# Kernel tuning notes

Measured on AMD Instinct MI355X. Metric: run time of the kernel, lower is better.

## Reference

```python
import jax, jax.numpy as jnp
import numpy as np

B, S, H, W, C = 1, 14, 56, 56, 192
WS = 7            # cubic window
SH = 3            # shift
HEADS = 6
HD = C // HEADS
N = WS ** 3       # 343 tokens per window
NW = (S // WS) * (H // WS) * (W // WS)  # 128 windows
SCALE = HD ** -0.5
HID = 4 * C
TBL = (2 * WS - 1) ** 3  # 2197


def _rel_index():
    # faithful to torch: meshgrid with indexing='xy' and the (3*ws-1)/(2*ws-1) strides
    c = np.stack(np.meshgrid(np.arange(WS), np.arange(WS), np.arange(WS), indexing='xy'))
    f = c.reshape(3, -1)                      # (3, N)
    r = (f[:, :, None] - f[:, None, :]).transpose(1, 2, 0)  # (N, N, 3)
    r = r + (WS - 1)
    r[..., 0] *= 3 * WS - 1
    r[..., 1] *= 2 * WS - 1
    return jnp.asarray(r.sum(-1), dtype=jnp.int32)  # (N, N)

REL_IDX = _rel_index()


def _ln(x, g, b):
    m = x.mean(-1, keepdims=True)
    v = ((x - m) ** 2).mean(-1, keepdims=True)
    return (x - m) * jax.lax.rsqrt(v + 1e-5) * g + b


def _partition(x):  # (B,S,H,W,C) -> (B*nW, N, C)
    x = x.reshape(B, S // WS, WS, H // WS, WS, W // WS, WS, C)
    x = x.transpose(0, 1, 3, 5, 2, 4, 6, 7)
    return x.reshape(-1, N, C)


def _reverse(w):  # (B*nW, N, C) -> (B,S,H,W,C)
    x = w.reshape(B, S // WS, H // WS, W // WS, WS, WS, WS, C)
    x = x.transpose(0, 1, 4, 2, 5, 3, 6, 7)
    return x.reshape(B, S, H, W, C)


def setup_inputs() -> dict:
    key = jax.random.key(0)
    ks = jax.random.split(key, 16)
    L = S * H * W
    p = lambda k, shp, s=0.02: (jax.random.normal(k, shp, dtype=jnp.float32) * s)
    return {
        'x': jax.random.normal(ks[0], (B, L, C), dtype=jnp.float32),
        'mask_matrix': jax.random.normal(ks[1], (NW, N, N), dtype=jnp.float32),
        'skip': jax.random.normal(ks[2], (B, L, C), dtype=jnp.float32),
        'x_up': jax.random.normal(ks[3], (B, L, C), dtype=jnp.float32),
        'norm1_g': jnp.ones((C,), jnp.float32),
        'norm1_b': jnp.zeros((C,), jnp.float32),
        'kv_w': p(ks[4], (C, 2 * C)),
        'kv_b': jnp.zeros((2 * C,), jnp.float32),
        'rel_bias_table': p(ks[5], (TBL, HEADS)),
        'proj_w': p(ks[6], (C, C)),
        'proj_b': jnp.zeros((C,), jnp.float32),
        'norm2_g': jnp.ones((C,), jnp.float32),
        'norm2_b': jnp.zeros((C,), jnp.float32),
        'fc1_w': p(ks[7], (C, HID)),
        'fc1_b': jnp.zeros((HID,), jnp.float32),
        'fc2_w': p(ks[8], (HID, C)),
        'fc2_b': jnp.zeros((C,), jnp.float32),
    }


def reference(x, mask_matrix, skip, x_up, norm1_g, norm1_b, kv_w, kv_b,
              rel_bias_table, proj_w, proj_b, norm2_g, norm2_b,
              fc1_w, fc1_b, fc2_w, fc2_b):
    shortcut = x
    sk = _ln(skip, norm1_g, norm1_b).reshape(B, S, H, W, C)
    xu = _ln(x_up, norm1_g, norm1_b).reshape(B, S, H, W, C)
    # cyclic shift (shift_size > 0, dims divisible by window -> no padding)
    sk = jnp.roll(sk, (-SH, -SH, -SH), axis=(1, 2, 3))
    xu = jnp.roll(xu, (-SH, -SH, -SH), axis=(1, 2, 3))
    sk_w = _partition(sk)   # (Bw, N, C)
    xu_w = _partition(xu)
    Bw = sk_w.shape[0]
    kv = (sk_w @ kv_w + kv_b).reshape(Bw, N, 2, HEADS, HD)
    k = kv[:, :, 0].transpose(0, 2, 1, 3)   # (Bw, h, N, d)
    v = kv[:, :, 1].transpose(0, 2, 1, 3)
    q = xu_w.reshape(Bw, N, HEADS, HD).transpose(0, 2, 1, 3) * SCALE
    attn = jnp.einsum('bhnd,bhmd->bhnm', q, k)
    bias = rel_bias_table[REL_IDX].transpose(2, 0, 1)  # (h, N, N)
    attn = attn + bias[None]
    attn = attn.reshape(B, NW, HEADS, N, N) + mask_matrix[None, :, None]
    attn = jax.nn.softmax(attn.reshape(Bw, HEADS, N, N), axis=-1)
    out = jnp.einsum('bhnm,bhmd->bhnd', attn, v)
    out = out.transpose(0, 2, 1, 3).reshape(Bw, N, C)
    out = out @ proj_w + proj_b
    xr = _reverse(out)
    xr = jnp.roll(xr, (SH, SH, SH), axis=(1, 2, 3)).reshape(B, S * H * W, C)
    x = shortcut + xr
    h = _ln(x, norm2_g, norm2_b)
    h = jax.nn.gelu(h @ fc1_w + fc1_b, approximate=False) @ fc2_w + fc2_b
    return x + h
```

## Files before the change

kernel.cpp:

```cpp
#include <hip/hip_runtime.h>
#include <cstddef>

typedef unsigned short u16;
typedef unsigned int   u32;
typedef __bf16 bf16_t;
typedef bf16_t bf16x8 __attribute__((ext_vector_type(8)));
typedef short  s16x4  __attribute__((ext_vector_type(4)));
typedef float  f32x4  __attribute__((ext_vector_type(4)));
typedef u16    u16x4  __attribute__((ext_vector_type(4)));

#define NPAD 352
#define VTS  352

__device__ __forceinline__ u16 f2b(float f) {
  return __builtin_bit_cast(u16, (__bf16)f);
}
__device__ __forceinline__ float b2f(u16 h) {
  return __uint_as_float(((u32)h) << 16);
}
__device__ __forceinline__ f32x4 mfma16(bf16x8 a, bf16x8 b, f32x4 c) {
  return __builtin_amdgcn_mfma_f32_16x16x32_bf16(a, b, c, 0, 0, 0);
}
__device__ __forceinline__ f32x4 mfma16x16(s16x4 a, s16x4 b, f32x4 c) {
#if __has_builtin(__builtin_amdgcn_mfma_f32_16x16x16bf16_1k)
  return __builtin_amdgcn_mfma_f32_16x16x16bf16_1k(a, b, c, 0, 0, 0);
#else
  f32x4 d;
  asm volatile("v_mfma_f32_16x16x16_bf16 %0, %1, %2, %3"
               : "=&v"(d) : "v"(a), "v"(b), "v"(c));
  return d;
#endif
}
__device__ __forceinline__ void gl_lds16(const void* g, void* l) {
  __builtin_amdgcn_global_load_lds((const __attribute__((address_space(1))) void*)g,
                                   (__attribute__((address_space(3))) void*)l, 16, 0, 0);
}

__device__ __forceinline__ int win_to_global(int w, int n) {
  int ws = w >> 6, wh = (w >> 3) & 7, ww = w & 7;
  int ts = (n * 1338) >> 16;
  int rem = n - ts * 49;
  int th = (rem * 9363) >> 16;
  int tw = rem - th * 7;
  int gs = ws * 7 + ts + 3; if (gs >= 14) gs -= 14;
  int gh = wh * 7 + th + 3; if (gh >= 56) gh -= 56;
  int gw = ww * 7 + tw + 3; if (gw >= 56) gw -= 56;
  return (gs * 56 + gh) * 56 + gw;
}

__global__ __launch_bounds__(256) void k_wconv(const float* __restrict__ kv_w,
    const float* __restrict__ proj_w, const float* __restrict__ fc1_w,
    const float* __restrict__ fc2_w, u16* kvT, u16* projT, u16* fc1T, u16* fc2T) {
  int t = blockIdx.x * 256 + threadIdx.x;
  if (t < 384 * 192) { int nn = t / 192, kk = t - nn * 192; kvT[t] = f2b(kv_w[kk * 384 + nn]); return; }
  t -= 384 * 192;
  if (t < 256 * 192) { int nn = t / 192, kk = t - nn * 192; projT[t] = (nn < 192) ? f2b(proj_w[kk * 192 + nn]) : (u16)0; return; }
  t -= 256 * 192;
  if (t < 768 * 192) { int nn = t / 192, kk = t - nn * 192; fc1T[t] = f2b(fc1_w[kk * 768 + nn]); return; }
  t -= 768 * 192;
  if (t < 256 * 768) { int nn = t / 768, kk = t - nn * 768; fc2T[t] = (nn < 192) ? f2b(fc2_w[kk * 192 + nn]) : (u16)0; return; }
}

__global__ __launch_bounds__(352) void k_bias(const float* __restrict__ tbl, u16* __restrict__ bf) {
  int m = threadIdx.x, n = blockIdx.x, h = blockIdx.y;
  u16 v = 0;
  if (n < 343 && m < 343) {
    int tsn = (n * 1338) >> 16, remn = n - tsn * 49, thn = (remn * 9363) >> 16, twn = remn - thn * 7;
    int tsm = (m * 1338) >> 16, remm = m - tsm * 49, thm = (remm * 9363) >> 16, twm = remm - thm * 7;
    int idx = (thn - thm) * 20 + (tsn - tsm) * 13 + (twn - twm) + 204;
    v = f2b(tbl[idx * 6 + h]);
  }
  bf[((size_t)h * 352 + n) * 352 + m] = v;
}

__global__ __launch_bounds__(256) void k_maskconv(const float* __restrict__ mask, u16* __restrict__ mb) {
  int t = blockIdx.x * 256 + threadIdx.x;
  int w = t / (352 * 88);
  int r = t - w * (352 * 88);
  int n = r / 88;
  int q = r - n * 88;
  u16x4 v = {0, 0, 0, 0};
  if (n < 343) {
    const float* src = mask + ((size_t)w * 343 + n) * 343 + q * 4;
    #pragma unroll
    for (int j = 0; j < 4; ++j) if (q * 4 + j < 343) v[j] = f2b(src[j]);
  }
  *(u16x4*)&mb[((size_t)w * 352 + n) * 352 + q * 4] = v;
}

__global__ __launch_bounds__(256) void k_ln1(const float* __restrict__ skip, const float* __restrict__ xup,
    const float* __restrict__ g1, const float* __restrict__ b1,
    u16* __restrict__ skw, u16* __restrict__ qb) {
  int wid = threadIdx.x >> 6, lane = threadIdx.x & 63;
  int m = blockIdx.x * 4 + wid;
  u32 w = ((u32)m * 48914u) >> 24;
  int n = m - (int)w * 343;
  int g = win_to_global((int)w, n);
  float xs[3], xu[3];
  float s1 = 0.f, s2 = 0.f, t1 = 0.f, t2 = 0.f;
  #pragma unroll
  for (int i = 0; i < 3; ++i) {
    int c = lane + i * 64;
    xs[i] = skip[(size_t)g * 192 + c];
    xu[i] = xup[(size_t)g * 192 + c];
    s1 += xs[i]; s2 += xs[i] * xs[i];
    t1 += xu[i]; t2 += xu[i] * xu[i];
  }
  #pragma unroll
  for (int off = 1; off < 64; off <<= 1) {
    s1 += __shfl_xor(s1, off); s2 += __shfl_xor(s2, off);
    t1 += __shfl_xor(t1, off); t2 += __shfl_xor(t2, off);
  }
  const float inv = 1.f / 192.f;
  float ms = s1 * inv, vs = s2 * inv - ms * ms;
  float mu = t1 * inv, vu = t2 * inv - mu * mu;
  float rs = rsqrtf(vs + 1e-5f), ru = rsqrtf(vu + 1e-5f);
  #pragma unroll
  for (int i = 0; i < 3; ++i) {
    int c = lane + i * 64;
    float gg = g1[c], bb = b1[c];
    skw[(size_t)m * 192 + c] = f2b((xs[i] - ms) * rs * gg + bb);
    float qv = ((xu[i] - mu) * ru * gg + bb) * 0.17677669529663687f;
    int h = c >> 5, d = c & 31;
    qb[(size_t)(((int)w * 6 + h) * NPAD + n) * 32 + d] = f2b(qv);
  }
}

__global__ __launch_bounds__(256) void k_ln2(const float* __restrict__ xr,
    const float* __restrict__ g2, const float* __restrict__ b2, u16* __restrict__ o) {
  int wid = threadIdx.x >> 6, lane = threadIdx.x & 63;
  int m = blockIdx.x * 4 + wid;
  float v[3]; float s1 = 0.f, s2 = 0.f;
  #pragma unroll
  for (int i = 0; i < 3; ++i) {
    int c = lane + i * 64;
    v[i] = xr[(size_t)m * 192 + c];
    s1 += v[i]; s2 += v[i] * v[i];
  }
  #pragma unroll
  for (int off = 1; off < 64; off <<= 1) { s1 += __shfl_xor(s1, off); s2 += __shfl_xor(s2, off); }
  const float inv = 1.f / 192.f;
  float ms = s1 * inv, vs = s2 * inv - ms * ms;
  float rs = rsqrtf(vs + 1e-5f);
  #pragma unroll
  for (int i = 0; i < 3; ++i) {
    int c = lane + i * 64;
    o[(size_t)m * 192 + c] = f2b((v[i] - ms) * rs * g2[c] + b2[c]);
  }
}

template<int EPI>
__global__ __launch_bounds__(256) void k_gemm(
    const u16* __restrict__ A, const u16* __restrict__ Bm, int K, int nbn,
    const float* __restrict__ bias,
    u16* __restrict__ outa, u16* __restrict__ outb,
    const float* __restrict__ xin, float* __restrict__ xres,
    float* __restrict__ outf) {
  __shared__ __align__(16) u16 As[128 * 32];
  __shared__ __align__(16) u16 Bs[128 * 32];
  int bid = blockIdx.x;
  int xcd = bid & 7, j = bid >> 3;
  int bn = j % nbn, bmL = j / nbn;
  int bm = xcd * 43 + bmL;
  if (bm >= 343) return;
  int tid = threadIdx.x;
  int wid = tid >> 6, lane = tid & 63, lr = lane & 15, lg = lane >> 4;
  int wr = wid >> 1, wc = wid & 1;
  f32x4 acc[4][4] = {};
  const u16* Abase = A + (size_t)bm * 128 * K;
  const u16* Bbase = Bm + (size_t)bn * 128 * K;
  int nk = K >> 5;
  for (int kt = 0; kt < nk; ++kt) {
    int ci0 = tid, ci1 = tid + 256;
    int r0 = ci0 >> 2, c0 = (ci0 & 3) * 8;
    int r1 = ci1 >> 2, c1 = (ci1 & 3) * 8;
    gl_lds16(Abase + (size_t)r0 * K + kt * 32 + c0, &As[ci0 * 8]);
    gl_lds16(Abase + (size_t)r1 * K + kt * 32 + c1, &As[ci1 * 8]);
    gl_lds16(Bbase + (size_t)r0 * K + kt * 32 + c0, &Bs[ci0 * 8]);
    gl_lds16(Bbase + (size_t)r1 * K + kt * 32 + c1, &Bs[ci1 * 8]);
    __syncthreads();
    bf16x8 af[4], bfr[4];
    #pragma unroll
    for (int mi = 0; mi < 4; ++mi) af[mi] = *(const bf16x8*)&As[(wr * 64 + mi * 16 + lr) * 32 + lg * 8];
    #pragma unroll
    for (int ni = 0; ni < 4; ++ni) bfr[ni] = *(const bf16x8*)&Bs[(wc * 64 + ni * 16 + lr) * 32 + lg * 8];
    #pragma unroll
    for (int mi = 0; mi < 4; ++mi)
      #pragma unroll
      for (int ni = 0; ni < 4; ++ni)
        acc[mi][ni] = mfma16(af[mi], bfr[ni], acc[mi][ni]);
    __syncthreads();
  }
  #pragma unroll
  for (int mi = 0; mi < 4; ++mi) {
    #pragma unroll
    for (int r = 0; r < 4; ++r) {
      int grow = bm * 128 + wr * 64 + mi * 16 + lg * 4 + r;
      if (EPI == 0) {
        u32 w = ((u32)grow * 48914u) >> 24; int n = grow - (int)w * 343;
        #pragma unroll
        for (int ni = 0; ni < 4; ++ni) {
          int gcol = bn * 128 + wc * 64 + ni * 16 + lr;
          float v = acc[mi][ni][r] + bias[gcol];
          if (gcol < 192) {
            int hh = gcol >> 5, d = gcol & 31;
            int dswz = ((((d >> 3) ^ ((n >> 1) & 3)) << 3) | (d & 7));
            outa[(size_t)(((int)w * 6 + hh) * NPAD + n) * 32 + dswz] = f2b(v);
          } else {
            int c2 = gcol - 192; int hh = c2 >> 5, d = c2 & 31;
            int nswz = ((((n >> 3) ^ ((d >> 1) & 3)) << 3) | (n & 7));
            outb[(size_t)(((int)w * 6 + hh) * 32 + d) * VTS + nswz] = f2b(v);
          }
        }
      } else if (EPI == 1) {
        #pragma unroll
        for (int ni = 0; ni < 4; ++ni) {
          int gcol = bn * 128 + wc * 64 + ni * 16 + lr;
          if (gcol < 192) {
            float v = acc[mi][ni][r] + bias[gcol] + xin[(size_t)grow * 192 + gcol];
            xres[(size_t)grow * 192 + gcol] = v;
          }
        }
      } else if (EPI == 2) {
        #pragma unroll
        for (int ni = 0; ni < 4; ++ni) {
          int gcol = bn * 128 + wc * 64 + ni * 16 + lr;
          float v = acc[mi][ni][r] + bias[gcol];
          v = 0.5f * v * (1.f + erff(v * 0.7071067811865476f));
          outa[(size_t)grow * 768 + gcol] = f2b(v);
        }
      } else {
        #pragma unroll
        for (int ni = 0; ni < 4; ++ni) {
          int gcol = bn * 128 + wc * 64 + ni * 16 + lr;
          if (gcol < 192)
            outf[(size_t)grow * 192 + gcol] = acc[mi][ni][r] + bias[gcol] + xin[(size_t)grow * 192 + gcol];
        }
      }
    }
  }
}

__global__ __launch_bounds__(256, 2) void k_attn(const u16* __restrict__ qb, const u16* __restrict__ kb,
    const u16* __restrict__ vtb, const u16* __restrict__ bfull, const u16* __restrict__ maskbf,
    u16* __restrict__ att) {
  __shared__ __align__(16) u16 Ks[352 * 32];
  __shared__ __align__(16) u16 Vs[32 * 352];
  __shared__ __align__(16) u16 Ot[4][16][40];
  int bid = blockIdx.x;
  int xcd = bid & 7, i = bid >> 3;
  int wl = i / 6, h = i - wl * 6;
  int w = xcd * 16 + wl;
  int tid = threadIdx.x, wid = tid >> 6, lane = tid & 63, lr = lane & 15, lg = lane >> 4;
  const u16* Q  = qb  + (size_t)(w * 6 + h) * NPAD * 32;
  const u16* Kg = kb  + (size_t)(w * 6 + h) * NPAD * 32;
  const u16* Vg = vtb + (size_t)(w * 6 + h) * 32 * VTS;
  const u16* Bp = bfull + (size_t)h * 352 * 352;
  const u16* Mp = maskbf + (size_t)w * 352 * 352;
  #pragma unroll
  for (int it = 0; it < 11; ++it) {
    int idx = it * 256 + tid;
    if (idx < 1408) gl_lds16(Kg + idx * 8, &Ks[idx * 8]);
    else            gl_lds16(Vg + (idx - 1408) * 8, &Vs[(idx - 1408) * 8]);
  }
  __syncthreads();
  int swz = (lr >> 1) & 3;
  for (int rt = wid; rt < 22; rt += 4) {
    int n = rt * 16 + lr;
    bf16x8 qa = *(const bf16x8*)&Q[(size_t)n * 32 + lg * 8];
    const u16* brow = Bp + (size_t)n * 352 + lg * 4;
    const u16* mrow = Mp + (size_t)n * 352 + lg * 4;
    f32x4 o0 = {0.f, 0.f, 0.f, 0.f}, o1 = {0.f, 0.f, 0.f, 0.f};
    float mrun = -1e30f, sum = 0.f;
    #pragma unroll
    for (int ch = 0; ch < 2; ++ch) {
      f32x4 s[11];
      #pragma unroll
      for (int j = 0; j < 11; ++j) {
        int ct = ch * 11 + j;
        u16x4 bb = *(const u16x4*)&brow[ct * 16];
        u16x4 mm = *(const u16x4*)&mrow[ct * 16];
        #pragma unroll
        for (int r = 0; r < 4; ++r) s[j][r] = b2f(bb[r]) + b2f(mm[r]);
      }
      #pragma unroll
      for (int j = 0; j < 11; ++j) {
        int ct = ch * 11 + j;
        bf16x8 kf = *(const bf16x8*)&Ks[(ct * 16 + lr) * 32 + (lg ^ swz) * 8];
        s[j] = mfma16(kf, qa, s[j]);
      }
      if (ch == 1) {
        int m0 = 336 + lg * 4;
        #pragma unroll
        for (int r = 0; r < 4; ++r) if (m0 + r >= 343) s[10][r] = -1e30f;
      }
      float mloc = -1e30f;
      #pragma unroll
      for (int j = 0; j < 11; ++j)
        mloc = fmaxf(mloc, fmaxf(fmaxf(s[j][0], s[j][1]), fmaxf(s[j][2], s[j][3])));
      mloc = fmaxf(mloc, __shfl_xor(mloc, 16));
      mloc = fmaxf(mloc, __shfl_xor(mloc, 32));
      float mnew = fmaxf(mrun, mloc);
      float scale = __expf(mrun - mnew);
      #pragma unroll
      for (int r = 0; r < 4; ++r) { o0[r] *= scale; o1[r] *= scale; }
      sum *= scale;
      float lsum = 0.f;
      #pragma unroll
      for (int j = 0; j < 11; ++j)
        #pragma unroll
        for (int r = 0; r < 4; ++r) { float p = __expf(s[j][r] - mnew); s[j][r] = p; lsum += p; }
      lsum += __shfl_xor(lsum, 16);
      lsum += __shfl_xor(lsum, 32);
      sum += lsum;
      mrun = mnew;
      #pragma unroll
      for (int j = 0; j < 11; ++j) {
        int ct = ch * 11 + j;
        s16x4 pa;
        #pragma unroll
        for (int r = 0; r < 4; ++r) pa[r] = (short)f2b(s[j][r]);
        int c16 = 2 * ct + (lg >> 1);
        int vo = ((c16 ^ swz) * 8) + (lg & 1) * 4;
        s16x4 v0 = *(const s16x4*)&Vs[lr * 352 + vo];
        s16x4 v1 = *(const s16x4*)&Vs[(16 + lr) * 352 + vo];
        o0 = mfma16x16(pa, v0, o0);
        o1 = mfma16x16(pa, v1, o1);
      }
    }
    float rs = 1.f / sum;
    #pragma unroll
    for (int r = 0; r < 4; ++r) {
      Ot[wid][lg * 4 + r][lr] = f2b(o0[r] * rs);
      Ot[wid][lg * 4 + r][16 + lr] = f2b(o1[r] * rs);
    }
    if (n < 343) {
      int g = win_to_global(w, n);
      bf16x8 ov = *(const bf16x8*)&Ot[wid][lr][lg * 8];
      *(bf16x8*)&att[(size_t)g * 192 + h * 32 + lg * 8] = ov;
    }
  }
}

static const size_t OFF_W    = 0;
static const size_t OFF_XRES = (size_t)1 << 20;
static const size_t OFF_MASK = OFF_XRES;
static const size_t OFF_LN2  = OFF_XRES + ((size_t)34 << 20);
static const size_t OFF_SKW  = OFF_LN2  + ((size_t)17 << 20);
static const size_t OFF_Q    = OFF_SKW  + ((size_t)17 << 20);
static const size_t OFF_K    = OFF_Q    + ((size_t)17 << 20);
static const size_t OFF_VT   = OFF_K    + ((size_t)17 << 20);
static const size_t OFF_ATT  = OFF_VT   + ((size_t)17 << 20);
static const size_t OFF_BIAS = OFF_ATT  + ((size_t)17 << 20);
static const size_t OFF_FC1  = OFF_SKW;

extern "C" void kernel_launch(void* const* d_in, const int* in_sizes, int n_in,
                              void* d_out, int out_size, void* d_ws, size_t ws_size,
                              hipStream_t stream) {
  const float* x      = (const float*)d_in[0];
  const float* mask   = (const float*)d_in[1];
  const float* skip   = (const float*)d_in[2];
  const float* xup    = (const float*)d_in[3];
  const float* n1g    = (const float*)d_in[4];
  const float* n1b    = (const float*)d_in[5];
  const float* kv_w   = (const float*)d_in[6];
  const float* kv_b   = (const float*)d_in[7];
  const float* tbl    = (const float*)d_in[8];
  const float* proj_w = (const float*)d_in[9];
  const float* proj_b = (const float*)d_in[10];
  const float* n2g    = (const float*)d_in[11];
  const float* n2b    = (const float*)d_in[12];
  const float* fc1_w  = (const float*)d_in[13];
  const float* fc1_b  = (const float*)d_in[14];
  const float* fc2_w  = (const float*)d_in[15];
  const float* fc2_b  = (const float*)d_in[16];
  char* ws = (char*)d_ws;
  u16* kvT   = (u16*)(ws + OFF_W);
  u16* projT = kvT + 384 * 192;
  u16* fc1T  = projT + 256 * 192;
  u16* fc2T  = fc1T + 768 * 192;
  float* xres = (float*)(ws + OFF_XRES);
  u16* maskbf = (u16*)(ws + OFF_MASK);
  u16* ln2o  = (u16*)(ws + OFF_LN2);
  u16* skw   = (u16*)(ws + OFF_SKW);
  u16* qb    = (u16*)(ws + OFF_Q);
  u16* kb    = (u16*)(ws + OFF_K);
  u16* vt    = (u16*)(ws + OFF_VT);
  u16* att   = (u16*)(ws + OFF_ATT);
  u16* bfull = (u16*)(ws + OFF_BIAS);
  u16* fc1o  = (u16*)(ws + OFF_FC1);
  float* outp = (float*)d_out;

  k_wconv<<<dim3(1824), dim3(256), 0, stream>>>(kv_w, proj_w, fc1_w, fc2_w, kvT, projT, fc1T, fc2T);
  k_bias<<<dim3(352, 6), dim3(352), 0, stream>>>(tbl, bfull);
  k_maskconv<<<dim3(15488), dim3(256), 0, stream>>>(mask, maskbf);
  k_ln1<<<dim3(10976), dim3(256), 0, stream>>>(skip, xup, n1g, n1b, skw, qb);
  k_gemm<0><<<dim3(8 * 43 * 3), dim3(256), 0, stream>>>(skw, kvT, 192, 3, kv_b, kb, vt, nullptr, nullptr, nullptr);
  k_attn<<<dim3(768), dim3(256), 0, stream>>>(qb, kb, vt, bfull, maskbf, att);
  k_gemm<1><<<dim3(8 * 43 * 2), dim3(256), 0, stream>>>(att, projT, 192, 2, proj_b, nullptr, nullptr, x, xres, nullptr);
  k_ln2<<<dim3(10976), dim3(256), 0, stream>>>(xres, n2g, n2b, ln2o);
  k_gemm<2><<<dim3(8 * 43 * 6), dim3(256), 0, stream>>>(ln2o, fc1T, 192, 6, fc1_b, fc1o, nullptr, nullptr, nullptr, nullptr);
  k_gemm<3><<<dim3(8 * 43 * 2), dim3(256), 0, stream>>>(fc1o, fc2T, 768, 2, fc2_b, nullptr, nullptr, xres, nullptr, outp);
}
```

Measured before the change: 344.2 us.

## Merge preprocessing kernels into one launch and software-pipeline attention bias loads

Folds the mask conversion, LN1, weight conversion and relative-bias expansion kernels into a single launch split by block range. This removes three launches and the idle gaps between them. The attention inner loop is rewritten into four chunks of 6/6/6/4 column tiles, with bias and mask loads issued one chunk ahead and s_setprio raised around the MFMA sections, so global-load latency can hide behind compute. The extra prefetch registers raise register pressure and could hurt occupancy at the two-blocks-per-SM launch bound.

```diff
diff --git a/kernel.cpp b/kernel.cpp
--- a/kernel.cpp
+++ b/kernel.cpp
@@ -48,81 +48,97 @@
   return (gs * 56 + gh) * 56 + gw;
 }
 
-__global__ __launch_bounds__(256) void k_wconv(const float* __restrict__ kv_w,
-    const float* __restrict__ proj_w, const float* __restrict__ fc1_w,
-    const float* __restrict__ fc2_w, u16* kvT, u16* projT, u16* fc1T, u16* fc2T) {
-  int t = blockIdx.x * 256 + threadIdx.x;
-  if (t < 384 * 192) { int nn = t / 192, kk = t - nn * 192; kvT[t] = f2b(kv_w[kk * 384 + nn]); return; }
-  t -= 384 * 192;
-  if (t < 256 * 192) { int nn = t / 192, kk = t - nn * 192; projT[t] = (nn < 192) ? f2b(proj_w[kk * 192 + nn]) : (u16)0; return; }
-  t -= 256 * 192;
-  if (t < 768 * 192) { int nn = t / 192, kk = t - nn * 192; fc1T[t] = f2b(fc1_w[kk * 768 + nn]); return; }
-  t -= 768 * 192;
-  if (t < 256 * 768) { int nn = t / 768, kk = t - nn * 768; fc2T[t] = (nn < 192) ? f2b(fc2_w[kk * 192 + nn]) : (u16)0; return; }
-}
-
-__global__ __launch_bounds__(352) void k_bias(const float* __restrict__ tbl, u16* __restrict__ bf) {
-  int m = threadIdx.x, n = blockIdx.x, h = blockIdx.y;
-  u16 v = 0;
-  if (n < 343 && m < 343) {
-    int tsn = (n * 1338) >> 16, remn = n - tsn * 49, thn = (remn * 9363) >> 16, twn = remn - thn * 7;
-    int tsm = (m * 1338) >> 16, remm = m - tsm * 49, thm = (remm * 9363) >> 16, twm = remm - thm * 7;
-    int idx = (thn - thm) * 20 + (tsn - tsm) * 13 + (twn - twm) + 204;
-    v = f2b(tbl[idx * 6 + h]);
-  }
-  bf[((size_t)h * 352 + n) * 352 + m] = v;
-}
-
-__global__ __launch_bounds__(256) void k_maskconv(const float* __restrict__ mask, u16* __restrict__ mb) {
-  int t = blockIdx.x * 256 + threadIdx.x;
-  int w = t / (352 * 88);
-  int r = t - w * (352 * 88);
-  int n = r / 88;
-  int q = r - n * 88;
-  u16x4 v = {0, 0, 0, 0};
-  if (n < 343) {
-    const float* src = mask + ((size_t)w * 343 + n) * 343 + q * 4;
-    #pragma unroll
-    for (int j = 0; j < 4; ++j) if (q * 4 + j < 343) v[j] = f2b(src[j]);
-  }
-  *(u16x4*)&mb[((size_t)w * 352 + n) * 352 + q * 4] = v;
-}
-
-__global__ __launch_bounds__(256) void k_ln1(const float* __restrict__ skip, const float* __restrict__ xup,
+#define MC_END 15488
+#define LN_END (MC_END + 10976)
+#define WC_END (LN_END + 1824)
+#define PRE_GRID (WC_END + 726)
+
+__global__ __launch_bounds__(256) void k_pre(
+    const float* __restrict__ mask, u16* __restrict__ mb,
+    const float* __restrict__ skip, const float* __restrict__ xup,
     const float* __restrict__ g1, const float* __restrict__ b1,
-    u16* __restrict__ skw, u16* __restrict__ qb) {
-  int wid = threadIdx.x >> 6, lane = threadIdx.x & 63;
-  int m = blockIdx.x * 4 + wid;
-  u32 w = ((u32)m * 48914u) >> 24;
-  int n = m - (int)w * 343;
-  int g = win_to_global((int)w, n);
-  float xs[3], xu[3];
-  float s1 = 0.f, s2 = 0.f, t1 = 0.f, t2 = 0.f;
-  #pragma unroll
-  for (int i = 0; i < 3; ++i) {
-    int c = lane + i * 64;
-    xs[i] = skip[(size_t)g * 192 + c];
-    xu[i] = xup[(size_t)g * 192 + c];
-    s1 += xs[i]; s2 += xs[i] * xs[i];
-    t1 += xu[i]; t2 += xu[i] * xu[i];
-  }
-  #pragma unroll
-  for (int off = 1; off < 64; off <<= 1) {
-    s1 += __shfl_xor(s1, off); s2 += __shfl_xor(s2, off);
-    t1 += __shfl_xor(t1, off); t2 += __shfl_xor(t2, off);
-  }
-  const float inv = 1.f / 192.f;
-  float ms = s1 * inv, vs = s2 * inv - ms * ms;
-  float mu = t1 * inv, vu = t2 * inv - mu * mu;
-  float rs = rsqrtf(vs + 1e-5f), ru = rsqrtf(vu + 1e-5f);
-  #pragma unroll
-  for (int i = 0; i < 3; ++i) {
-    int c = lane + i * 64;
-    float gg = g1[c], bb = b1[c];
-    skw[(size_t)m * 192 + c] = f2b((xs[i] - ms) * rs * gg + bb);
-    float qv = ((xu[i] - mu) * ru * gg + bb) * 0.17677669529663687f;
-    int h = c >> 5, d = c & 31;
-    qb[(size_t)(((int)w * 6 + h) * NPAD + n) * 32 + d] = f2b(qv);
+    u16* __restrict__ skw, u16* __restrict__ qb,
+    const float* __restrict__ kv_w, const float* __restrict__ proj_w,
+    const float* __restrict__ fc1_w, const float* __restrict__ fc2_w,
+    u16* kvT, u16* projT, u16* fc1T, u16* fc2T,
+    const float* __restrict__ tbl, u16* __restrict__ bf) {
+  int bid = blockIdx.x, tid = threadIdx.x;
+  if (bid < MC_END) {
+    int t = bid * 256 + tid;
+    int w = t / (352 * 88);
+    int r = t - w * (352 * 88);
+    int n = r / 88;
+    int q = r - n * 88;
+    u16x4 v = {0, 0, 0, 0};
+    if (n < 343) {
+      const float* src = mask + ((size_t)w * 343 + n) * 343 + q * 4;
+      #pragma unroll
+      for (int j = 0; j < 4; ++j) if (q * 4 + j < 343) v[j] = f2b(src[j]);
+    }
+    *(u16x4*)&mb[((size_t)w * 352 + n) * 352 + q * 4] = v;
+  } else if (bid < LN_END) {
+    int wid = tid >> 6, lane = tid & 63;
+    int m = (bid - MC_END) * 4 + wid;
+    u32 w = ((u32)m * 48914u) >> 24;
+    int n = m - (int)w * 343;
+    int g = win_to_global((int)w, n);
+    float xs[3], xu[3];
+    float s1 = 0.f, s2 = 0.f, t1 = 0.f, t2 = 0.f;
+    #pragma unroll
+    for (int i = 0; i < 3; ++i) {
+      int c = lane + i * 64;
+      xs[i] = skip[(size_t)g * 192 + c];
+      xu[i] = xup[(size_t)g * 192 + c];
+      s1 += xs[i]; s2 += xs[i] * xs[i];
+      t1 += xu[i]; t2 += xu[i] * xu[i];
+    }
+    #pragma unroll
+    for (int off = 1; off < 64; off <<= 1) {
+      s1 += __shfl_xor(s1, off); s2 += __shfl_xor(s2, off);
+      t1 += __shfl_xor(t1, off); t2 += __shfl_xor(t2, off);
+    }
+    const float inv = 1.f / 192.f;
+    float ms = s1 * inv, vs = s2 * inv - ms * ms;
+    float mu = t1 * inv, vu = t2 * inv - mu * mu;
+    float rs = rsqrtf(vs + 1e-5f), ru = rsqrtf(vu + 1e-5f);
+    #pragma unroll
+    for (int i = 0; i < 3; ++i) {
+      int c = lane + i * 64;
+      float gg = g1[c], bb = b1[c];
+      skw[(size_t)m * 192 + c] = f2b((xs[i] - ms) * rs * gg + bb);
+      float qv = ((xu[i] - mu) * ru * gg + bb) * 0.17677669529663687f;
+      int h = c >> 5, d = c & 31;
+      qb[(size_t)(((int)w * 6 + h) * NPAD + n) * 32 + d] = f2b(qv);
+    }
+  } else if (bid < WC_END) {
+    int t = (bid - LN_END) * 256 + tid;
+    if (t < 384 * 192) { int nn = t / 192, kk = t - nn * 192; kvT[t] = f2b(kv_w[kk * 384 + nn]); return; }
+    t -= 384 * 192;
+    if (t < 256 * 192) { int nn = t / 192, kk = t - nn * 192; projT[t] = (nn < 192) ? f2b(proj_w[kk * 192 + nn]) : (u16)0; return; }
+    t -= 256 * 192;
+    if (t < 768 * 192) { int nn = t / 192, kk = t - nn * 192; fc1T[t] = f2b(fc1_w[kk * 768 + nn]); return; }
+    t -= 768 * 192;
+    if (t < 256 * 768) { int nn = t / 768, kk = t - nn * 768; fc2T[t] = (nn < 192) ? f2b(fc2_w[kk * 192 + nn]) : (u16)0; return; }
+  } else {
+    int t = (bid - WC_END) * 256 + tid;
+    int h = t / (352 * 88);
+    int r = t - h * (352 * 88);
+    int n = r / 88;
+    int q = r - n * 88;
+    u16x4 v = {0, 0, 0, 0};
+    if (n < 343 && h < 6) {
+      int tsn = (n * 1338) >> 16, remn = n - tsn * 49, thn = (remn * 9363) >> 16, twn = remn - thn * 7;
+      #pragma unroll
+      for (int j = 0; j < 4; ++j) {
+        int m = q * 4 + j;
+        if (m < 343) {
+          int tsm = (m * 1338) >> 16, remm = m - tsm * 49, thm = (remm * 9363) >> 16, twm = remm - thm * 7;
+          int idx = (thn - thm) * 20 + (tsn - tsm) * 13 + (twn - twm) + 204;
+          v[j] = f2b(tbl[idx * 6 + h]);
+        }
+      }
+    }
+    if (h < 6) *(u16x4*)&bf[((size_t)h * 352 + n) * 352 + q * 4] = v;
   }
 }
 
@@ -241,6 +257,74 @@
   }
 }
 
+template<int CT0, int LEN>
+__device__ __forceinline__ void pf_load(const u16* __restrict__ brow, const u16* __restrict__ mrow,
+                                        u16x4* bb, u16x4* mm) {
+  #pragma unroll
+  for (int j = 0; j < LEN; ++j) {
+    bb[j] = *(const u16x4*)&brow[(CT0 + j) * 16];
+    mm[j] = *(const u16x4*)&mrow[(CT0 + j) * 16];
+  }
+}
+
+template<int CT0, int LEN, bool TAIL>
+__device__ __forceinline__ void attn_chunk(const u16* __restrict__ Ks, const u16* __restrict__ Vs,
+    bf16x8 qa, int lr, int lg, int swz, const u16x4* bb, const u16x4* mm,
+    f32x4& o0, f32x4& o1, float& mrun, float& sum) {
+  f32x4 s[LEN];
+  const f32x4 z = {0.f, 0.f, 0.f, 0.f};
+  __builtin_amdgcn_s_setprio(1);
+  #pragma unroll
+  for (int j = 0; j < LEN; ++j) {
+    bf16x8 kf = *(const bf16x8*)&Ks[((CT0 + j) * 16 + lr) * 32 + (lg ^ swz) * 8];
+    s[j] = mfma16(kf, qa, z);
+  }
+  __builtin_amdgcn_s_setprio(0);
+  #pragma unroll
+  for (int j = 0; j < LEN; ++j)
+    #pragma unroll
+    for (int r = 0; r < 4; ++r) s[j][r] += b2f(bb[j][r]) + b2f(mm[j][r]);
+  if (TAIL) {
+    int m0 = 336 + lg * 4;
+    #pragma unroll
+    for (int r = 0; r < 4; ++r) if (m0 + r >= 343) s[LEN - 1][r] = -1e30f;
+  }
+  float mloc = -1e30f;
+  #pragma unroll
+  for (int j = 0; j < LEN; ++j)
+    mloc = fmaxf(mloc, fmaxf(fmaxf(s[j][0], s[j][1]), fmaxf(s[j][2], s[j][3])));
+  mloc = fmaxf(mloc, __shfl_xor(mloc, 16));
+  mloc = fmaxf(mloc, __shfl_xor(mloc, 32));
+  float mnew = fmaxf(mrun, mloc);
+  float scale = __expf(mrun - mnew);
+  #pragma unroll
+  for (int r = 0; r < 4; ++r) { o0[r] *= scale; o1[r] *= scale; }
+  sum *= scale;
+  float lsum = 0.f;
+  #pragma unroll
+  for (int j = 0; j < LEN; ++j)
+    #pragma unroll
+    for (int r = 0; r < 4; ++r) { float p = __expf(s[j][r] - mnew); s[j][r] = p; lsum += p; }
+  lsum += __shfl_xor(lsum, 16);
+  lsum += __shfl_xor(lsum, 32);
+  sum += lsum;
+  mrun = mnew;
+  __builtin_amdgcn_s_setprio(1);
+  #pragma unroll
+  for (int j = 0; j < LEN; ++j) {
+    s16x4 pa;
+    #pragma unroll
+    for (int r = 0; r < 4; ++r) pa[r] = (short)f2b(s[j][r]);
+    int c16 = 2 * (CT0 + j) + (lg >> 1);
+    int vo = ((c16 ^ swz) * 8) + (lg & 1) * 4;
+    s16x4 v0 = *(const s16x4*)&Vs[lr * 352 + vo];
+    s16x4 v1 = *(const s16x4*)&Vs[(16 + lr) * 352 + vo];
+    o0 = mfma16x16(pa, v0, o0);
+    o1 = mfma16x16(pa, v1, o1);
+  }
+  __builtin_amdgcn_s_setprio(0);
+}
+
 __global__ __launch_bounds__(256, 2) void k_attn(const u16* __restrict__ qb, const u16* __restrict__ kb,
     const u16* __restrict__ vtb, const u16* __restrict__ bfull, const u16* __restrict__ maskbf,
     u16* __restrict__ att) {
@@ -272,62 +356,15 @@
     const u16* mrow = Mp + (size_t)n * 352 + lg * 4;
     f32x4 o0 = {0.f, 0.f, 0.f, 0.f}, o1 = {0.f, 0.f, 0.f, 0.f};
     float mrun = -1e30f, sum = 0.f;
-    #pragma unroll
-    for (int ch = 0; ch < 2; ++ch) {
-      f32x4 s[11];
-      #pragma unroll
-      for (int j = 0; j < 11; ++j) {
-        int ct = ch * 11 + j;
-        u16x4 bb = *(const u16x4*)&brow[ct * 16];
-        u16x4 mm = *(const u16x4*)&mrow[ct * 16];
-        #pragma unroll
-        for (int r = 0; r < 4; ++r) s[j][r] = b2f(bb[r]) + b2f(mm[r]);
-      }
-      #pragma unroll
-      for (int j = 0; j < 11; ++j) {
-        int ct = ch * 11 + j;
-        bf16x8 kf = *(const bf16x8*)&Ks[(ct * 16 + lr) * 32 + (lg ^ swz) * 8];
-        s[j] = mfma16(kf, qa, s[j]);
-      }
-      if (ch == 1) {
-        int m0 = 336 + lg * 4;
-        #pragma unroll
-        for (int r = 0; r < 4; ++r) if (m0 + r >= 343) s[10][r] = -1e30f;
-      }
-      float mloc = -1e30f;
-      #pragma unroll
-      for (int j = 0; j < 11; ++j)
-        mloc = fmaxf(mloc, fmaxf(fmaxf(s[j][0], s[j][1]), fmaxf(s[j][2], s[j][3])));
-      mloc = fmaxf(mloc, __shfl_xor(mloc, 16));
-      mloc = fmaxf(mloc, __shfl_xor(mloc, 32));
-      float mnew = fmaxf(mrun, mloc);
-      float scale = __expf(mrun - mnew);
-      #pragma unroll
-      for (int r = 0; r < 4; ++r) { o0[r] *= scale; o1[r] *= scale; }
-      sum *= scale;
-      float lsum = 0.f;
-      #pragma unroll
-      for (int j = 0; j < 11; ++j)
-        #pragma unroll
-        for (int r = 0; r < 4; ++r) { float p = __expf(s[j][r] - mnew); s[j][r] = p; lsum += p; }
-      lsum += __shfl_xor(lsum, 16);
-      lsum += __shfl_xor(lsum, 32);
-      sum += lsum;
-      mrun = mnew;
-      #pragma unroll
-      for (int j = 0; j < 11; ++j) {
-        int ct = ch * 11 + j;
-        s16x4 pa;
-        #pragma unroll
-        for (int r = 0; r < 4; ++r) pa[r] = (short)f2b(s[j][r]);
-        int c16 = 2 * ct + (lg >> 1);
-        int vo = ((c16 ^ swz) * 8) + (lg & 1) * 4;
-        s16x4 v0 = *(const s16x4*)&Vs[lr * 352 + vo];
-        s16x4 v1 = *(const s16x4*)&Vs[(16 + lr) * 352 + vo];
-        o0 = mfma16x16(pa, v0, o0);
-        o1 = mfma16x16(pa, v1, o1);
-      }
-    }
+    u16x4 bbA[6], mmA[6], bbB[6], mmB[6];
+    pf_load<0, 6>(brow, mrow, bbA, mmA);
+    pf_load<6, 6>(brow, mrow, bbB, mmB);
+    attn_chunk<0, 6, false>(Ks, Vs, qa, lr, lg, swz, bbA, mmA, o0, o1, mrun, sum);
+    pf_load<12, 6>(brow, mrow, bbA, mmA);
+    attn_chunk<6, 6, false>(Ks, Vs, qa, lr, lg, swz, bbB, mmB, o0, o1, mrun, sum);
+    pf_load<18, 4>(brow, mrow, bbB, mmB);
+    attn_chunk<12, 6, false>(Ks, Vs, qa, lr, lg, swz, bbA, mmA, o0, o1, mrun, sum);
+    attn_chunk<18, 4, true>(Ks, Vs, qa, lr, lg, swz, bbB, mmB, o0, o1, mrun, sum);
     float rs = 1.f / sum;
     #pragma unroll
     for (int r = 0; r < 4; ++r) {
@@ -391,10 +428,9 @@
   u16* fc1o  = (u16*)(ws + OFF_FC1);
   float* outp = (float*)d_out;
 
-  k_wconv<<<dim3(1824), dim3(256), 0, stream>>>(kv_w, proj_w, fc1_w, fc2_w, kvT, projT, fc1T, fc2T);
-  k_bias<<<dim3(352, 6), dim3(352), 0, stream>>>(tbl, bfull);
-  k_maskconv<<<dim3(15488), dim3(256), 0, stream>>>(mask, maskbf);
-  k_ln1<<<dim3(10976), dim3(256), 0, stream>>>(skip, xup, n1g, n1b, skw, qb);
+  k_pre<<<dim3(PRE_GRID), dim3(256), 0, stream>>>(
+      mask, maskbf, skip, xup, n1g, n1b, skw, qb,
+      kv_w, proj_w, fc1_w, fc2_w, kvT, projT, fc1T, fc2T, tbl, bfull);
   k_gemm<0><<<dim3(8 * 43 * 3), dim3(256), 0, stream>>>(skw, kvT, 192, 3, kv_b, kb, vt, nullptr, nullptr, nullptr);
   k_attn<<<dim3(768), dim3(256), 0, stream>>>(qb, kb, vt, bfull, maskbf, att);
   k_gemm<1><<<dim3(8 * 43 * 2), dim3(256), 0, stream>>>(att, projT, 192, 2, proj_b, nullptr, nullptr, x, xres, nullptr);
```

Result: faster. 317.9 us (-7.6%).
